# Optimization experiments

Measured on AMD Instinct MI355X. Metric: run time of the kernel, lower is better.

The kernel has to match this reference:

```python
import jax, jax.numpy as jnp
import numpy as np

H = 16        # query heads
HK = 8        # key/value heads
HD = 128      # head dim
EPS = 1e-6
THETA = 1000000.0


def _rmsnorm(x, w):
    # per-head RMSNorm over last dim (head_dim)
    var = jnp.mean(jnp.square(x.astype(jnp.float32)), axis=-1, keepdims=True)
    return (x * jax.lax.rsqrt(var + EPS)).astype(x.dtype) * w


def _rope(x, cos, sin):
    # x: [B, S, h, HD]; cos/sin: [S, HD//2]
    x1, x2 = jnp.split(x, 2, axis=-1)
    c = cos[None, :, None, :]
    s = sin[None, :, None, :]
    return jnp.concatenate([x1 * c - x2 * s, x2 * c + x1 * s], axis=-1)


def setup_inputs() -> dict:
    key = jax.random.key(0)
    ks = jax.random.split(key, 5)
    B, S, D = 2, 2048, 2048
    scale = 0.02
    return {
        "x": jax.random.normal(ks[0], (B, S, D), jnp.float32),
        "wq": jax.random.normal(ks[1], (H * HD, D), jnp.float32) * scale,
        "wk": jax.random.normal(ks[2], (HK * HD, D), jnp.float32) * scale,
        "wv": jax.random.normal(ks[3], (HK * HD, D), jnp.float32) * scale,
        "wo": jax.random.normal(ks[4], (D, H * HD), jnp.float32) * scale,
        "q_norm_w": jnp.ones((HD,), jnp.float32),
        "k_norm_w": jnp.ones((HD,), jnp.float32),
    }


def reference(x, wq, wk, wv, wo, q_norm_w, k_norm_w):
    B, S, D = x.shape
    # QKV projections (no bias)
    q = (x @ wq.T).reshape(B, S, H, HD)
    k = (x @ wk.T).reshape(B, S, HK, HD)
    v = (x @ wv.T).reshape(B, S, HK, HD)

    # per-head RMSNorm on Q and K (Qwen3 qk-norm)
    q = _rmsnorm(q, q_norm_w)
    k = _rmsnorm(k, k_norm_w)

    # RoPE
    inv_freq = 1.0 / (THETA ** (jnp.arange(0, HD, 2, dtype=jnp.float32) / HD))
    ang = jnp.arange(S, dtype=jnp.float32)[:, None] * inv_freq[None, :]  # [S, HD/2]
    cos, sin = jnp.cos(ang), jnp.sin(ang)
    q = _rope(q, cos, sin)
    k = _rope(k, cos, sin)

    # GQA: repeat KV heads to match query heads
    rep = H // HK
    k = jnp.repeat(k, rep, axis=2)  # [B, S, H, HD]
    v = jnp.repeat(v, rep, axis=2)

    # causal SDPA
    scores = jnp.einsum("bqhd,bkhd->bhqk", q, k) / jnp.sqrt(jnp.float32(HD))
    mask = jnp.tril(jnp.ones((S, S), dtype=bool))
    scores = jnp.where(mask[None, None], scores, jnp.finfo(scores.dtype).min)
    probs = jax.nn.softmax(scores, axis=-1)
    out = jnp.einsum("bhqk,bkhd->bqhd", probs, v).reshape(B, S, H * HD)

    return out @ wo.T
```

## Files before the change

### kernel.cpp

```cpp
#include <hip/hip_runtime.h>
#include <hip/hip_bf16.h>
#include <math.h>

#define B_   2
#define S_   2048
#define D_   2048
#define H_   16
#define HK_  8
#define HD_  128
#define BS_  (B_ * S_)
#define NQKV 4096
#define SCALE 0.08838834764831845f

typedef __bf16 bf16x8 __attribute__((ext_vector_type(8)));
typedef __bf16 bf16x4 __attribute__((ext_vector_type(4)));
typedef float  f32x4  __attribute__((ext_vector_type(4)));

#define AS1(p) ((const __attribute__((address_space(1))) void*)(p))
#define AS3(p) ((__attribute__((address_space(3))) void*)(p))

template <int S>
__device__ __forceinline__ float ror16(float x) {
    return __builtin_bit_cast(float, __builtin_amdgcn_update_dpp(
        0, __builtin_bit_cast(int, x), 0x120 | S, 0xF, 0xF, true));
}
__device__ __forceinline__ float row_sum16(float x) {
    x += ror16<8>(x);
    x += ror16<4>(x);
    x += ror16<2>(x);
    x += ror16<1>(x);
    return x;
}

__global__ __launch_bounds__(256) void cvt_all(const float* __restrict__ x,
                                               const float* __restrict__ wq,
                                               const float* __restrict__ wk,
                                               const float* __restrict__ wv,
                                               const float* __restrict__ wo,
                                               __bf16* __restrict__ xb,
                                               __bf16* __restrict__ wb,
                                               __bf16* __restrict__ wob) {
    int bid = blockIdx.x;
    const float* src;
    __bf16* dst;
    int i4;
    if (bid < 8192)       { src = x;  dst = xb;                    i4 = bid * 256; }
    else if (bid < 12288) { src = wq; dst = wb;                    i4 = (bid - 8192) * 256; }
    else if (bid < 14336) { src = wk; dst = wb + (size_t)4194304;  i4 = (bid - 12288) * 256; }
    else if (bid < 16384) { src = wv; dst = wb + (size_t)6291456;  i4 = (bid - 14336) * 256; }
    else                  { src = wo; dst = wob;                   i4 = (bid - 16384) * 256; }
    i4 += threadIdx.x;
    float4 v = reinterpret_cast<const float4*>(src)[i4];
    bf16x4 o = {(__bf16)v.x, (__bf16)v.y, (__bf16)v.z, (__bf16)v.w};
    reinterpret_cast<bf16x4*>(dst)[i4] = o;
}

__global__ __launch_bounds__(128) void build_rope(float* __restrict__ tab) {
    int s = blockIdx.x;
    int d = threadIdx.x;
    int i = d & 63;
    float inv_freq = exp2f(-19.931568569324174f * (float)(2 * i) * (1.0f / 128.0f));
    float ang = (float)s * inv_freq;
    float sn, cs;
    sincosf(ang, &sn, &cs);
    tab[s * 128 + d] = (d < 64) ? cs : sn;
}

__global__ __launch_bounds__(512, 2) void gemm_bf16_8ph(const __bf16* __restrict__ A,
                                                        const __bf16* __restrict__ W,
                                                        __bf16* __restrict__ C,
                                                        int M, int N, int K) {
    __shared__ __bf16 lds[2][2][256 * 64];

    const int t    = threadIdx.x;
    const int w    = t >> 6;
    const int lane = t & 63;
    const int col  = lane & 15;
    const int quad = lane >> 4;
    const int c7   = col & 7;
    const int wm   = w >> 2;
    const int wn   = w & 3;

    const int m0 = blockIdx.y * 256;
    const int n0 = blockIdx.x * 256;

    const int lr8 = lane >> 3;
    const int sw8 = ((lane & 7) ^ lr8) * 8;
    const __bf16* Ag = A + (size_t)(m0 + w * 16 + lr8) * K + sw8;
    const __bf16* Wg = W + (size_t)(n0 + w * 16 + lr8) * K + sw8;

    const int nkt = K >> 6;
    const int nit = nkt >> 1;

    const int aBase = (wm * 128 + col) * 64;
    const int bBase = (wn * 64 + col) * 64;
    const int kx0 = (quad ^ c7) * 8;
    const int kx1 = ((4 + quad) ^ c7) * 8;

    f32x4 acc[8][4];
    #pragma unroll
    for (int i = 0; i < 8; i++)
        #pragma unroll
        for (int j = 0; j < 4; j++) acc[i][j] = (f32x4){0.f, 0.f, 0.f, 0.f};

    bf16x8 a[4][2], a2[4][2], b[2][2];

    auto stg = [&](int ktv, int bufc, int ab, int half) {
        if (ktv >= nkt) return;
        const __bf16* gb = (ab ? Wg : Ag) + (size_t)half * 128 * K + (size_t)ktv * 64;
        __bf16* db = &lds[bufc][ab][(half * 128 + w * 16) * 64];
        __builtin_amdgcn_global_load_lds(AS1(gb), AS3(db), 16, 0, 0);
        __builtin_amdgcn_global_load_lds(AS1(gb + (size_t)8 * K), AS3(db + 512), 16, 0, 0);
    };
    auto lda = [&](bf16x8 (&dst)[4][2], const __bf16* panel, int g) {
        #pragma unroll
        for (int mi = 0; mi < 4; mi++) {
            dst[mi][0] = *reinterpret_cast<const bf16x8*>(&panel[aBase + (g * 64 + mi * 16) * 64 + kx0]);
            dst[mi][1] = *reinterpret_cast<const bf16x8*>(&panel[aBase + (g * 64 + mi * 16) * 64 + kx1]);
        }
    };
    auto ldb = [&](const __bf16* panel, int ng) {
        #pragma unroll
        for (int ni = 0; ni < 2; ni++) {
            b[ni][0] = *reinterpret_cast<const bf16x8*>(&panel[bBase + (ng * 32 + ni * 16) * 64 + kx0]);
            b[ni][1] = *reinterpret_cast<const bf16x8*>(&panel[bBase + (ng * 32 + ni * 16) * 64 + kx1]);
        }
    };
    auto mm = [&](bf16x8 (&af)[4][2], int g, int ng) {
        __builtin_amdgcn_s_setprio(1);
        #pragma unroll
        for (int mi = 0; mi < 4; mi++)
            #pragma unroll
            for (int ni = 0; ni < 2; ni++) {
                f32x4 c = acc[g * 4 + mi][ng * 2 + ni];
                c = __builtin_amdgcn_mfma_f32_16x16x32_bf16(af[mi][0], b[ni][0], c, 0, 0, 0);
                c = __builtin_amdgcn_mfma_f32_16x16x32_bf16(af[mi][1], b[ni][1], c, 0, 0, 0);
                acc[g * 4 + mi][ng * 2 + ni] = c;
            }
        __builtin_amdgcn_s_setprio(0);
    };

#define BARS do { __builtin_amdgcn_s_barrier(); __builtin_amdgcn_sched_barrier(0); } while (0)
#define LGKM0 asm volatile("s_waitcnt lgkmcnt(0)" ::: "memory")

    stg(0, 0, 0, 0); stg(0, 0, 0, 1); stg(0, 0, 1, 0); stg(0, 0, 1, 1);
    stg(1, 1, 0, 0); stg(1, 1, 0, 1);
    asm volatile("s_waitcnt vmcnt(4)" ::: "memory");
    BARS;

    #pragma unroll 1
    for (int it = 0; it < nit; ++it) {
        const int k2 = it * 2;
        const bool last = (it == nit - 1);

        const __bf16* A0p = &lds[0][0][0];
        const __bf16* B0p = &lds[0][1][0];
        const __bf16* A1p = &lds[1][0][0];
        const __bf16* B1p = &lds[1][1][0];

        lda(a, A0p, 0); ldb(B0p, 0);
        stg(k2 + 1, 1, 1, 0);
        BARS; LGKM0;
        mm(a, 0, 0);
        BARS;
        lda(a2, A0p, 1);
        stg(k2 + 1, 1, 1, 1);
        BARS; LGKM0;
        mm(a2, 1, 0);
        BARS;
        ldb(B0p, 1);
        stg(k2 + 2, 0, 0, 0);
        BARS; LGKM0;
        mm(a, 0, 1);
        BARS;
        stg(k2 + 2, 0, 0, 1);
        BARS;
        mm(a2, 1, 1);
        if (last) { asm volatile("s_waitcnt vmcnt(0)" ::: "memory"); }
        else      { asm volatile("s_waitcnt vmcnt(4)" ::: "memory"); }
        BARS;

        lda(a, A1p, 0); ldb(B1p, 0);
        stg(k2 + 2, 0, 1, 0);
        BARS; LGKM0;
        mm(a, 0, 0);
        BARS;
        lda(a2, A1p, 1);
        stg(k2 + 2, 0, 1, 1);
        BARS; LGKM0;
        mm(a2, 1, 0);
        BARS;
        ldb(B1p, 1);
        stg(k2 + 3, 1, 0, 0);
        BARS; LGKM0;
        mm(a, 0, 1);
        BARS;
        stg(k2 + 3, 1, 0, 1);
        BARS;
        mm(a2, 1, 1);
        if (!last) { asm volatile("s_waitcnt vmcnt(4)" ::: "memory"); }
        BARS;
    }

#undef BARS
#undef LGKM0

    #pragma unroll
    for (int m8 = 0; m8 < 8; m8++) {
        #pragma unroll
        for (int r = 0; r < 4; r++) {
            size_t row = m0 + wm * 128 + m8 * 16 + quad * 4 + r;
            __bf16* cp = C + row * N + n0 + wn * 64 + col;
            #pragma unroll
            for (int n4 = 0; n4 < 4; n4++) cp[n4 * 16] = (__bf16)acc[m8][n4][r];
        }
    }
}

template <typename CT>
__global__ __launch_bounds__(256) void gemm_bf16_nt_n64(const __bf16* __restrict__ A,
                                                        const __bf16* __restrict__ W,
                                                        CT* __restrict__ C,
                                                        int M, int N, int K) {
    __shared__ __bf16 As[128 * 64];
    __shared__ __bf16 Bs[64 * 64];

    const int t    = threadIdx.x;
    const int w    = t >> 6;
    const int lane = t & 63;
    const int col  = lane & 15;
    const int quad = lane >> 4;
    const int wm   = w >> 1;
    const int wn   = w & 1;

    const int m0 = blockIdx.x * 128;
    const int n0 = blockIdx.y * 64;

    const int lrow8 = lane >> 3;
    const int lch   = ((lane & 7) ^ lrow8) * 8;

    const __bf16* agp = A + (size_t)(m0 + w * 32 + lrow8) * K + lch;
    const __bf16* wgp = W + (size_t)(n0 + w * 16 + lrow8) * K + lch;
    __bf16* alp = As + (w * 32) * 64;
    __bf16* blp = Bs + (w * 16) * 64;

    const int c7 = col & 7;

    f32x4 acc[4][2];
    #pragma unroll
    for (int m = 0; m < 4; m++)
        #pragma unroll
        for (int n = 0; n < 2; n++) acc[m][n] = (f32x4){0.f, 0.f, 0.f, 0.f};

    #pragma unroll 1
    for (int k0 = 0; k0 < K; k0 += 64) {
        #pragma unroll
        for (int j = 0; j < 4; j++)
            __builtin_amdgcn_global_load_lds(AS1(agp + k0 + (size_t)(j * 8) * K),
                                             AS3(alp + j * 512), 16, 0, 0);
        #pragma unroll
        for (int j = 0; j < 2; j++)
            __builtin_amdgcn_global_load_lds(AS1(wgp + k0 + (size_t)(j * 8) * K),
                                             AS3(blp + j * 512), 16, 0, 0);
        __syncthreads();

        #pragma unroll
        for (int kk = 0; kk < 2; kk++) {
            bf16x8 af[4], bfr[2];
            #pragma unroll
            for (int m = 0; m < 4; m++)
                af[m] = *reinterpret_cast<const bf16x8*>(
                    &As[(wm * 64 + m * 16 + col) * 64 + ((kk * 4 + quad) ^ c7) * 8]);
            #pragma unroll
            for (int n = 0; n < 2; n++)
                bfr[n] = *reinterpret_cast<const bf16x8*>(
                    &Bs[(wn * 32 + n * 16 + col) * 64 + ((kk * 4 + quad) ^ c7) * 8]);

            #pragma unroll
            for (int m = 0; m < 4; m++)
                #pragma unroll
                for (int n = 0; n < 2; n++)
                    acc[m][n] = __builtin_amdgcn_mfma_f32_16x16x32_bf16(af[m], bfr[n], acc[m][n], 0, 0, 0);
        }
        __syncthreads();
    }

    #pragma unroll
    for (int m = 0; m < 4; m++) {
        #pragma unroll
        for (int r = 0; r < 4; r++) {
            size_t row = m0 + wm * 64 + m * 16 + quad * 4 + r;
            CT* cp = C + row * N + n0 + wn * 32 + col;
            #pragma unroll
            for (int n = 0; n < 2; n++) cp[n * 16] = (CT)acc[m][n][r];
        }
    }
}

__global__ __launch_bounds__(256) void norm_rope(__bf16* __restrict__ qkv,
                                                 const float* __restrict__ qw,
                                                 const float* __restrict__ kw,
                                                 const float* __restrict__ tab) {
    const int g    = blockIdx.x * 16 + (threadIdx.x >> 4);
    const int l    = threadIdx.x & 15;
    const int row  = g / 24;
    const int head = g - row * 24;
    const int s    = row & (S_ - 1);

    const float* w = (head < H_) ? qw : kw;
    __bf16* p = qkv + (size_t)row * NQKV + head * HD_ + l * 8;

    bf16x8 xv = *reinterpret_cast<const bf16x8*>(p);
    float xf[8];
    float ss = 0.f;
    #pragma unroll
    for (int j = 0; j < 8; j++) { xf[j] = (float)xv[j]; ss = fmaf(xf[j], xf[j], ss); }
    ss = row_sum16(ss);
    float rs = rsqrtf(ss * (1.0f / 128.0f) + 1e-6f);

    float nf[8];
    const float4 w0 = *reinterpret_cast<const float4*>(&w[l * 8]);
    const float4 w1 = *reinterpret_cast<const float4*>(&w[l * 8 + 4]);
    nf[0] = xf[0] * rs * w0.x; nf[1] = xf[1] * rs * w0.y;
    nf[2] = xf[2] * rs * w0.z; nf[3] = xf[3] * rs * w0.w;
    nf[4] = xf[4] * rs * w1.x; nf[5] = xf[5] * rs * w1.y;
    nf[6] = xf[6] * rs * w1.z; nf[7] = xf[7] * rs * w1.w;

    float of[8];
    #pragma unroll
    for (int j = 0; j < 8; j++) of[j] = __shfl_xor(nf[j], 8);

    const int ib = (l & 7) * 8;
    const float4 c0 = *reinterpret_cast<const float4*>(&tab[s * 128 + ib]);
    const float4 c1 = *reinterpret_cast<const float4*>(&tab[s * 128 + ib + 4]);
    const float4 s0 = *reinterpret_cast<const float4*>(&tab[s * 128 + 64 + ib]);
    const float4 s1 = *reinterpret_cast<const float4*>(&tab[s * 128 + 64 + ib + 4]);
    float cs[8] = {c0.x, c0.y, c0.z, c0.w, c1.x, c1.y, c1.z, c1.w};
    float sn[8] = {s0.x, s0.y, s0.z, s0.w, s1.x, s1.y, s1.z, s1.w};

    bf16x8 out;
    if (l < 8) {
        #pragma unroll
        for (int j = 0; j < 8; j++) out[j] = (__bf16)(nf[j] * cs[j] - of[j] * sn[j]);
    } else {
        #pragma unroll
        for (int j = 0; j < 8; j++) out[j] = (__bf16)(of[j] * sn[j] + nf[j] * cs[j]);
    }
    *reinterpret_cast<bf16x8*>(p) = out;
}

__global__ __launch_bounds__(256) void transpose_v(const __bf16* __restrict__ qkv,
                                                   __bf16* __restrict__ vt) {
    __shared__ __bf16 Ls[64][136];
    const int t  = threadIdx.x;
    const int bk = blockIdx.y;
    const int b  = bk >> 3;
    const int kvh = bk & 7;
    const int s0 = blockIdx.x * 64;

    #pragma unroll
    for (int i = 0; i < 4; i++) {
        int f = t + i * 256;
        int row = f >> 4;
        int d8 = (f & 15) * 8;
        bf16x8 v = *reinterpret_cast<const bf16x8*>(
            &qkv[(size_t)(b * S_ + s0 + row) * NQKV + 3072 + kvh * HD_ + d8]);
        *reinterpret_cast<bf16x8*>(&Ls[row][d8]) = v;
    }
    __syncthreads();

    #pragma unroll
    for (int i = 0; i < 4; i++) {
        int f = t + i * 256;
        int dim = f >> 3;
        int kc = f & 7;
        bf16x8 o;
        #pragma unroll
        for (int e = 0; e < 8; e++) o[e] = Ls[kc * 8 + e][dim];
        *reinterpret_cast<bf16x8*>(
            &vt[((size_t)bk * HD_ + dim) * S_ + s0 + kc * 8]) = o;
    }
}

__global__ __launch_bounds__(256) void attn_mfma(const __bf16* __restrict__ qkv,
                                                 const __bf16* __restrict__ vt,
                                                 __bf16* __restrict__ ao) {
    __shared__ __align__(16) char smem[17408];
    __bf16 (*Qs)[136] = reinterpret_cast<__bf16(*)[136]>(smem);
    __bf16 (*Ks)[136] = reinterpret_cast<__bf16(*)[136]>(smem);
    __shared__ __bf16 Vt[128][72];
    __shared__ __bf16 Ps[4][16][72];

    const int t    = threadIdx.x;
    const int w    = t >> 6;
    const int lane = t & 63;
    const int col  = lane & 15;
    const int quad = lane >> 4;

    const int bh  = blockIdx.x;
    const int b   = bh >> 4;
    const int h   = bh & 15;
    const int kvh = h >> 1;
    const int qb  = gridDim.y - 1 - blockIdx.y;
    const int r0  = qb * 64;

    const float C0 = SCALE * 1.44269504f;
    const float CM = -12.0f * 1.44269504f;

    const __bf16* vbase = vt + ((size_t)(b * HK_ + kvh) * HD_) * S_;

    const __bf16* kp[4];
    __bf16*       kw_[4];
    const __bf16* vp[4];
    __bf16*       vw_[4];
    #pragma unroll
    for (int i = 0; i < 4; i++) {
        int f = t + i * 256;
        int row = f >> 4, d8 = (f & 15) * 8;
        kp[i]  = qkv + (size_t)(b * S_ + row) * NQKV + 2048 + kvh * HD_ + d8;
        kw_[i] = &Ks[row][d8];
        int dim = f >> 3, kc = f & 7;
        vp[i]  = vbase + (size_t)dim * S_ + kc * 8;
        vw_[i] = &Vt[dim][kc * 8];
    }

    bf16x8 kreg[4], vreg[4];
    #pragma unroll
    for (int i = 0; i < 4; i++) {
        kreg[i] = *reinterpret_cast<const bf16x8*>(kp[i]);  kp[i] += (size_t)64 * NQKV;
        vreg[i] = *reinterpret_cast<const bf16x8*>(vp[i]);  vp[i] += 64;
    }

    #pragma unroll
    for (int i = 0; i < 4; i++) {
        int f   = t + i * 256;
        int row = f >> 4;
        int d8  = (f & 15) * 8;
        bf16x8 v = *reinterpret_cast<const bf16x8*>(
            &qkv[(size_t)(b * S_ + r0 + row) * NQKV + h * HD_ + d8]);
        *reinterpret_cast<bf16x8*>(&Qs[row][d8]) = v;
    }
    __syncthreads();

    bf16x8 qf[4];
    {
        const int m = w * 16 + col;
        #pragma unroll
        for (int k = 0; k < 4; k++)
            qf[k] = *reinterpret_cast<const bf16x8*>(&Qs[m][k * 32 + quad * 8]);
    }

    f32x4 o_acc[8];
    #pragma unroll
    for (int i = 0; i < 8; i++) o_acc[i] = (f32x4){0.f, 0.f, 0.f, 0.f};
    float l_lane[4] = {0.f, 0.f, 0.f, 0.f};

    const int ntiles = qb + 1;
    for (int ti = 0; ti < ntiles; ti++) {
        __syncthreads();

        #pragma unroll
        for (int i = 0; i < 4; i++) {
            *reinterpret_cast<bf16x8*>(kw_[i]) = kreg[i];
            *reinterpret_cast<bf16x8*>(vw_[i]) = vreg[i];
        }
        if (ti + 1 < ntiles) {
            #pragma unroll
            for (int i = 0; i < 4; i++) {
                kreg[i] = *reinterpret_cast<const bf16x8*>(kp[i]);  kp[i] += (size_t)64 * NQKV;
                vreg[i] = *reinterpret_cast<const bf16x8*>(vp[i]);  vp[i] += 64;
            }
        }
        __syncthreads();

        f32x4 s[4];
        #pragma unroll
        for (int n = 0; n < 4; n++) {
            f32x4 acc = (f32x4){0.f, 0.f, 0.f, 0.f};
            #pragma unroll
            for (int k = 0; k < 4; k++) {
                bf16x8 bf = *reinterpret_cast<const bf16x8*>(
                    &Ks[n * 16 + col][k * 32 + quad * 8]);
                acc = __builtin_amdgcn_mfma_f32_16x16x32_bf16(qf[k], bf, acc, 0, 0, 0);
            }
            s[n] = acc;
        }

        const bool diag = (ti == qb);
        #pragma unroll
        for (int r = 0; r < 4; r++) {
            float p0 = exp2f(fmaf(s[0][r], C0, CM));
            float p1 = exp2f(fmaf(s[1][r], C0, CM));
            float p2 = exp2f(fmaf(s[2][r], C0, CM));
            float p3 = exp2f(fmaf(s[3][r], C0, CM));
            if (diag) {
                int qloc = w * 16 + quad * 4 + r;
                if (0 * 16 + col > qloc) p0 = 0.f;
                if (1 * 16 + col > qloc) p1 = 0.f;
                if (2 * 16 + col > qloc) p2 = 0.f;
                if (3 * 16 + col > qloc) p3 = 0.f;
            }
            l_lane[r] += p0 + p1 + p2 + p3;
            Ps[w][quad * 4 + r][0 * 16 + col] = (__bf16)p0;
            Ps[w][quad * 4 + r][1 * 16 + col] = (__bf16)p1;
            Ps[w][quad * 4 + r][2 * 16 + col] = (__bf16)p2;
            Ps[w][quad * 4 + r][3 * 16 + col] = (__bf16)p3;
        }

        bf16x8 pf[2];
        #pragma unroll
        for (int ks = 0; ks < 2; ks++)
            pf[ks] = *reinterpret_cast<const bf16x8*>(&Ps[w][col][ks * 32 + quad * 8]);
        #pragma unroll
        for (int n = 0; n < 8; n++) {
            #pragma unroll
            for (int ks = 0; ks < 2; ks++) {
                bf16x8 vf = *reinterpret_cast<const bf16x8*>(
                    &Vt[n * 16 + col][ks * 32 + quad * 8]);
                o_acc[n] = __builtin_amdgcn_mfma_f32_16x16x32_bf16(pf[ks], vf, o_acc[n], 0, 0, 0);
            }
        }
    }

    #pragma unroll
    for (int r = 0; r < 4; r++) {
        float l = row_sum16(l_lane[r]);
        float inv = 1.0f / l;
        int qrow = r0 + w * 16 + quad * 4 + r;
        __bf16* op = ao + (size_t)(b * S_ + qrow) * (H_ * HD_) + h * HD_ + col;
        #pragma unroll
        for (int n = 0; n < 8; n++)
            op[n * 16] = (__bf16)(o_acc[n][r] * inv);
    }
}

extern "C" void kernel_launch(void* const* d_in, const int* in_sizes, int n_in,
                              void* d_out, int out_size, void* d_ws, size_t ws_size,
                              hipStream_t stream) {
    const float* x  = (const float*)d_in[0];
    const float* wq = (const float*)d_in[1];
    const float* wk = (const float*)d_in[2];
    const float* wv = (const float*)d_in[3];
    const float* wo = (const float*)d_in[4];
    const float* qw = (const float*)d_in[5];
    const float* kw = (const float*)d_in[6];
    float* out = (float*)d_out;

    __bf16* ws  = (__bf16*)d_ws;
    __bf16* xb  = ws;
    __bf16* wb  = xb  + (size_t)8388608;
    __bf16* wob = wb  + (size_t)8388608;
    __bf16* qkv = wob + (size_t)4194304;
    __bf16* ao  = qkv + (size_t)16777216;
    __bf16* vtg = ao  + (size_t)8388608;
    float* rtab = (float*)ao;

    cvt_all<<<20480, 256, 0, stream>>>(x, wq, wk, wv, wo, xb, wb, wob);
    build_rope<<<S_, 128, 0, stream>>>(rtab);

    gemm_bf16_8ph<<<dim3(NQKV / 256, BS_ / 256), 512, 0, stream>>>(
        xb, wb, qkv, BS_, NQKV, D_);

    norm_rope<<<(BS_ * 24) / 16, 256, 0, stream>>>(qkv, qw, kw, rtab);

    transpose_v<<<dim3(S_ / 64, B_ * HK_), 256, 0, stream>>>(qkv, vtg);

    attn_mfma<<<dim3(B_ * H_, S_ / 64), 256, 0, stream>>>(qkv, vtg, ao);

    gemm_bf16_nt_n64<float><<<dim3(BS_ / 128, D_ / 64), 256, 0, stream>>>(
        ao, wob, out, BS_, D_, H_ * HD_);
}
```

Measured before the change: 335.1 us.

## Remap QKV GEMM blocks for XCD/L2 locality and trim pipeline barriers

The QKV GEMM now uses a 1-D grid of 256 blocks. Each block ID is remapped so consecutive IDs within an XCD cover a 4x4 supertile of output tiles, which should improve L2 reuse of A and W panels. The main loop also drops the extra barrier after each MFMA phase and moves the vmcnt wait ahead of the final barrier, which reduces synchronization per k-step. The risk is that the fewer barriers could allow LDS write/read races if the stage ordering was relying on them.

Result: no change. 341.6 us (+2.0%).

```diff
diff --git a/kernel.cpp b/kernel.cpp
--- a/kernel.cpp
+++ b/kernel.cpp
@@ -81,8 +81,12 @@
     const int wm   = w >> 2;
     const int wn   = w & 3;
 
-    const int m0 = blockIdx.y * 256;
-    const int n0 = blockIdx.x * 256;
+    const int bid = blockIdx.x;
+    const int nid = (bid & 7) * 32 + (bid >> 3);
+    const int st  = nid >> 4;
+    const int wi  = nid & 15;
+    const int m0 = ((st >> 2) * 4 + (wi >> 2)) * 256;
+    const int n0 = ((st & 3) * 4 + (wi & 3)) * 256;
 
     const int lr8 = lane >> 3;
     const int sw8 = ((lane & 7) ^ lr8) * 8;
@@ -140,13 +144,15 @@
         __builtin_amdgcn_s_setprio(0);
     };
 
-#define BARS do { __builtin_amdgcn_s_barrier(); __builtin_amdgcn_sched_barrier(0); } while (0)
-#define LGKM0 asm volatile("s_waitcnt lgkmcnt(0)" ::: "memory")
+#define BAR  __builtin_amdgcn_s_barrier()
+#define LGKM0 do { asm volatile("s_waitcnt lgkmcnt(0)" ::: "memory"); \
+                   __builtin_amdgcn_sched_barrier(0); } while (0)
+#define VM(n) asm volatile("s_waitcnt vmcnt(" #n ")" ::: "memory")
 
     stg(0, 0, 0, 0); stg(0, 0, 0, 1); stg(0, 0, 1, 0); stg(0, 0, 1, 1);
     stg(1, 1, 0, 0); stg(1, 1, 0, 1);
-    asm volatile("s_waitcnt vmcnt(4)" ::: "memory");
-    BARS;
+    VM(4);
+    BAR;
 
     #pragma unroll 1
     for (int it = 0; it < nit; ++it) {
@@ -160,50 +166,42 @@
 
         lda(a, A0p, 0); ldb(B0p, 0);
         stg(k2 + 1, 1, 1, 0);
-        BARS; LGKM0;
+        BAR; LGKM0;
         mm(a, 0, 0);
-        BARS;
         lda(a2, A0p, 1);
         stg(k2 + 1, 1, 1, 1);
-        BARS; LGKM0;
+        BAR; LGKM0;
         mm(a2, 1, 0);
-        BARS;
         ldb(B0p, 1);
         stg(k2 + 2, 0, 0, 0);
-        BARS; LGKM0;
+        BAR; LGKM0;
         mm(a, 0, 1);
-        BARS;
         stg(k2 + 2, 0, 0, 1);
-        BARS;
+        if (last) VM(0); else VM(4);
+        BAR;
         mm(a2, 1, 1);
-        if (last) { asm volatile("s_waitcnt vmcnt(0)" ::: "memory"); }
-        else      { asm volatile("s_waitcnt vmcnt(4)" ::: "memory"); }
-        BARS;
 
         lda(a, A1p, 0); ldb(B1p, 0);
         stg(k2 + 2, 0, 1, 0);
-        BARS; LGKM0;
+        BAR; LGKM0;
         mm(a, 0, 0);
-        BARS;
         lda(a2, A1p, 1);
         stg(k2 + 2, 0, 1, 1);
-        BARS; LGKM0;
+        BAR; LGKM0;
         mm(a2, 1, 0);
-        BARS;
         ldb(B1p, 1);
         stg(k2 + 3, 1, 0, 0);
-        BARS; LGKM0;
+        BAR; LGKM0;
         mm(a, 0, 1);
-        BARS;
         stg(k2 + 3, 1, 0, 1);
-        BARS;
+        if (!last) { VM(4); }
+        BAR;
         mm(a2, 1, 1);
-        if (!last) { asm volatile("s_waitcnt vmcnt(4)" ::: "memory"); }
-        BARS;
-    }
-
-#undef BARS
+    }
+
+#undef BAR
 #undef LGKM0
+#undef VM
 
     #pragma unroll
     for (int m8 = 0; m8 < 8; m8++) {
@@ -558,8 +556,7 @@
     cvt_all<<<20480, 256, 0, stream>>>(x, wq, wk, wv, wo, xb, wb, wob);
     build_rope<<<S_, 128, 0, stream>>>(rtab);
 
-    gemm_bf16_8ph<<<dim3(NQKV / 256, BS_ / 256), 512, 0, stream>>>(
-        xb, wb, qkv, BS_, NQKV, D_);
+    gemm_bf16_8ph<<<256, 512, 0, stream>>>(xb, wb, qkv, BS_, NQKV, D_);
 
     norm_rope<<<(BS_ * 24) / 16, 256, 0, stream>>>(qkv, qw, kw, rtab);
 
```
